# Kernel tuning notes

Measured on AMD Instinct MI355X. Metric: run time of the kernel, lower is better.

## Reference

```python
import jax, jax.numpy as jnp
import numpy as np

B, D_IN, D_H, N = 16, 32, 64, 4000
ORDER = 2
C_CAT = D_IN + D_H            # 96 channels into each gate conv
C_EFF = (ORDER + 1) * C_CAT   # 288 after order-K diffusion concat


def setup_inputs() -> dict:
    key = jax.random.key(0)
    ks = jax.random.split(key, 9)
    x = jax.random.normal(ks[0], (B, D_IN, N), dtype=jnp.float32)
    h = jax.random.normal(ks[1], (B, D_H, N), dtype=jnp.float32)
    # uniform adjacency, roughly row-normalized to keep diffusion stable
    adj = jax.random.uniform(ks[2], (N, N), dtype=jnp.float32) / N
    scale = 0.05
    Wf = jax.random.normal(ks[3], (D_H, C_EFF), dtype=jnp.float32) * scale
    Wu = jax.random.normal(ks[4], (D_H, C_EFF), dtype=jnp.float32) * scale
    Wc = jax.random.normal(ks[5], (D_H, C_EFF), dtype=jnp.float32) * scale
    bf = jax.random.normal(ks[6], (D_H,), dtype=jnp.float32) * scale
    bu = jax.random.normal(ks[7], (D_H,), dtype=jnp.float32) * scale
    bc = jax.random.normal(ks[8], (D_H,), dtype=jnp.float32) * scale
    return {"x": x, "h": h, "adj": adj, "Wf": Wf, "bf": bf,
            "Wu": Wu, "bu": bu, "Wc": Wc, "bc": bc}


def _spatial_conv(z, adj, W, b):
    # z: [b, c, n]; order-2 diffusion: concat [z, A z, A^2 z] then 1x1 conv
    z1 = jnp.einsum('mn,bcn->bcm', adj, z)
    z2 = jnp.einsum('mn,bcn->bcm', adj, z1)
    feats = jnp.concatenate([z, z1, z2], axis=1)           # [b, 3c, n]
    return jnp.einsum('oc,bcn->bon', W, feats) + b[None, :, None]


def reference(x, h, adj, Wf, bf, Wu, bu, Wc, bc):
    x_gates = jnp.concatenate([x, h], axis=1)              # [b, d_in+d_h, n]
    r = jax.nn.sigmoid(_spatial_conv(x_gates, adj, Wf, bf))
    u = jax.nn.sigmoid(_spatial_conv(x_gates, adj, Wu, bu))
    x_c = jnp.concatenate([x, r * h], axis=1)
    c = jnp.tanh(_spatial_conv(x_c, adj, Wc, bc))
    return u * h + (1.0 - u) * c
```

## Files before the change

kernel.cpp:

```cpp
#include <hip/hip_runtime.h>
#include <cstdint>


#define NREAL 4000
#define NPAD  4096

typedef unsigned short u16;
typedef __attribute__((ext_vector_type(8))) short short8;
typedef __attribute__((ext_vector_type(4))) float f32x4;
typedef __attribute__((ext_vector_type(4))) unsigned short u16x4;

__device__ __forceinline__ u16 f2bf(float f) {
  unsigned u = __builtin_bit_cast(unsigned, f);
  return (u16)((u + 0x7FFFu + ((u >> 16) & 1u)) >> 16);
}
__device__ __forceinline__ float bf2f(u16 b) {
  unsigned u = ((unsigned)b) << 16;
  return __builtin_bit_cast(float, u);
}

__global__ __launch_bounds__(256) void k_pack_adj(const float* __restrict__ adj,
                                                  u16* __restrict__ out) {
  const int idx = blockIdx.x * 256 + threadIdx.x;
  const int m = idx >> 10;
  const int n0 = (idx & 1023) << 2;
  u16x4 o;
  if (m < NREAL && n0 < NREAL) {
    const float4 v = *reinterpret_cast<const float4*>(&adj[(long)m * NREAL + n0]);
    o.x = f2bf(v.x); o.y = f2bf(v.y); o.z = f2bf(v.z); o.w = f2bf(v.w);
  } else {
    o.x = 0; o.y = 0; o.z = 0; o.w = 0;
  }
  *reinterpret_cast<u16x4*>(&out[(long)m * NPAD + n0]) = o;
}

__global__ __launch_bounds__(256) void k_pack_zg(const float* __restrict__ x,
                                                 const float* __restrict__ h,
                                                 u16* __restrict__ zg) {
  const int idx = blockIdx.x * 256 + threadIdx.x;
  const int row = idx >> 10;
  const int n0 = (idx & 1023) << 2;
  const int b = row / 96, c = row % 96;
  const float* src = (c < 32) ? &x[((long)b * 32 + c) * NREAL]
                              : &h[((long)b * 64 + (c - 32)) * NREAL];
  u16x4 o;
  if (n0 < NREAL) {
    const float4 v = *reinterpret_cast<const float4*>(&src[n0]);
    o.x = f2bf(v.x); o.y = f2bf(v.y); o.z = f2bf(v.z); o.w = f2bf(v.w);
  } else {
    o.x = 0; o.y = 0; o.z = 0; o.w = 0;
  }
  *reinterpret_cast<u16x4*>(&zg[(long)row * NPAD + n0]) = o;
}

__global__ __launch_bounds__(256) void k_pack_w(const float* __restrict__ Wf,
                                                const float* __restrict__ Wu,
                                                const float* __restrict__ Wc,
                                                float* __restrict__ Wgt,
                                                float* __restrict__ Wct) {
  const int idx = blockIdx.x * 256 + threadIdx.x;
  if (idx < 288 * 128) {
    const int c = idx >> 7, o = idx & 127;
    Wgt[idx] = (o < 64) ? Wf[o * 288 + c] : Wu[(o - 64) * 288 + c];
  }
  if (idx < 288 * 64) {
    const int c = idx >> 6, o = idx & 63;
    Wct[idx] = Wc[o * 288 + c];
  }
}

template<bool F32OUT>
__global__ __launch_bounds__(512, 2) void k_gemm256(const u16* __restrict__ A,
                                                    const u16* __restrict__ B,
                                                    void* __restrict__ Cout,
                                                    int ktPerChunk, long chunkElems) {
  __shared__ __align__(16) u16 As[2][256 * 64];
  __shared__ __align__(16) u16 Bs[2][256 * 64];
  const int tid = threadIdx.x;
  const int lane = tid & 63;
  const int wv = tid >> 6;
  const int wm = wv >> 2;
  const int wn = wv & 3;
  const int bm = blockIdx.y, bn = blockIdx.x;

  const int srow = tid >> 3;
  const int jlog = (tid & 7) ^ (srow & 7);
  const long kt0ofs = (long)blockIdx.z * ktPerChunk * 64;
  const u16* aS = A + (long)(bm * 256 + srow) * NPAD + kt0ofs + jlog * 8;
  const u16* bS = B + (long)(bn * 256 + srow) * NPAD + kt0ofs + jlog * 8;
  const int ldst = tid * 8;

  const int fr = lane & 15;
  const int ksub2 = ((lane >> 4) << 3) << 1;

  f32x4 acc[8][4] = {};

#define STAGE(buf, kk)                                                           \
  {                                                                              \
    const long ko = (long)(kk) * 64;                                             \
    _Pragma("unroll")                                                            \
    for (int i = 0; i < 4; ++i)                                                  \
      __builtin_amdgcn_global_load_lds(                                          \
          (const __attribute__((address_space(1))) void*)(aS + (long)i * 64 * NPAD + ko), \
          (__attribute__((address_space(3))) void*)(&As[buf][i * 4096 + ldst]), 16, 0, 0); \
    _Pragma("unroll")                                                            \
    for (int i = 0; i < 4; ++i)                                                  \
      __builtin_amdgcn_global_load_lds(                                          \
          (const __attribute__((address_space(1))) void*)(bS + (long)i * 64 * NPAD + ko), \
          (__attribute__((address_space(3))) void*)(&Bs[buf][i * 4096 + ldst]), 16, 0, 0); \
  }

  STAGE(0, 0)
  int cur = 0;
  for (int kk = 0; kk < ktPerChunk; ++kk) {
    if (kk + 1 < ktPerChunk) {
      STAGE(cur ^ 1, kk + 1)
      asm volatile("s_waitcnt vmcnt(8)\ns_barrier" ::: "memory");
    } else {
      asm volatile("s_waitcnt vmcnt(0)\ns_barrier" ::: "memory");
    }
    const char* Ab = (const char*)&As[cur][0];
    const char* Bb = (const char*)&Bs[cur][0];
#pragma unroll
    for (int ks = 0; ks < 2; ++ks) {
      const int k2 = (ks << 6) + ksub2;
      short8 av[8], bv[4];
#pragma unroll
      for (int mi = 0; mi < 8; ++mi) {
        const int row = (wm << 7) + (mi << 4) + fr;
        av[mi] = *(const short8*)(Ab + row * 128 + (k2 ^ ((row & 7) << 4)));
      }
#pragma unroll
      for (int ni = 0; ni < 4; ++ni) {
        const int row = (wn << 6) + (ni << 4) + fr;
        bv[ni] = *(const short8*)(Bb + row * 128 + (k2 ^ ((row & 7) << 4)));
      }
      __builtin_amdgcn_s_setprio(1);
#pragma unroll
      for (int mi = 0; mi < 8; ++mi)
#pragma unroll
        for (int ni = 0; ni < 4; ++ni)
          acc[mi][ni] = __builtin_amdgcn_mfma_f32_16x16x32_bf16(av[mi], bv[ni],
                                                                acc[mi][ni], 0, 0, 0);
      __builtin_amdgcn_s_setprio(0);
    }
    asm volatile("s_barrier" ::: "memory");
    cur ^= 1;
  }
#undef STAGE

  const int rb = bm * 256 + (wm << 7) + ((lane >> 4) << 2);
  const int cb = bn * 256 + (wn << 6) + fr;
  if (F32OUT) {
    float* C = (float*)Cout + (long)blockIdx.z * chunkElems;
#pragma unroll
    for (int mi = 0; mi < 8; ++mi)
#pragma unroll
      for (int ni = 0; ni < 4; ++ni)
#pragma unroll
        for (int q = 0; q < 4; ++q)
          C[(long)(rb + (mi << 4) + q) * NPAD + cb + (ni << 4)] = acc[mi][ni][q];
  } else {
    u16* C = (u16*)Cout;
#pragma unroll
    for (int mi = 0; mi < 8; ++mi)
#pragma unroll
      for (int ni = 0; ni < 4; ++ni)
#pragma unroll
        for (int q = 0; q < 4; ++q)
          C[(long)(rb + (mi << 4) + q) * NPAD + cb + (ni << 4)] = f2bf(acc[mi][ni][q]);
  }
}

template<int NC>
__global__ __launch_bounds__(256) void k_combine(const float* __restrict__ P,
                                                 long chunkElems,
                                                 u16* __restrict__ out) {
  const long i4 = ((long)blockIdx.x * 256 + threadIdx.x) * 4;
  f32x4 s = *reinterpret_cast<const f32x4*>(&P[i4]);
#pragma unroll
  for (int c = 1; c < NC; ++c) {
    const f32x4 v = *reinterpret_cast<const f32x4*>(&P[(long)c * chunkElems + i4]);
    s.x += v.x; s.y += v.y; s.z += v.z; s.w += v.w;
  }
  u16x4 o;
  o.x = f2bf(s.x); o.y = f2bf(s.y); o.z = f2bf(s.z); o.w = f2bf(s.w);
  *reinterpret_cast<u16x4*>(&out[i4]) = o;
}

__global__ __launch_bounds__(512) void k_gates(
    const float* __restrict__ x, const float* __restrict__ h,
    const float* __restrict__ Wgt,
    const float* __restrict__ bfv, const float* __restrict__ buv,
    const u16* __restrict__ Z1, const u16* __restrict__ Z2,
    u16* __restrict__ rh_bf, float* __restrict__ rh_f, float* __restrict__ u_f) {
  const int lane = threadIdx.x & 63;
  const int wq = __builtin_amdgcn_readfirstlane(threadIdx.x >> 6);
  const int b = blockIdx.y;
  const int n0 = blockIdx.x * 128 + (lane << 1);
  if (n0 >= NREAL) return;
  const int ob = wq << 4;
  const float* xb = x + (long)b * 32 * NREAL + n0;
  const float* hb = h + (long)b * 64 * NREAL + n0;
  const u16* z1b = Z1 + (long)b * 96 * NPAD + n0;
  const u16* z2b = Z2 + (long)b * 96 * NPAD + n0;

  float a0[16] = {}, a1[16] = {};
#pragma unroll 4
  for (int c = 0; c < 32; ++c) {
    const float2 f = *reinterpret_cast<const float2*>(&xb[(long)c * NREAL]);
#pragma unroll
    for (int oi = 0; oi < 16; ++oi) {
      const float w = Wgt[c * 128 + ob + oi];
      a0[oi] = fmaf(w, f.x, a0[oi]); a1[oi] = fmaf(w, f.y, a1[oi]);
    }
  }
#pragma unroll 4
  for (int c = 0; c < 64; ++c) {
    const float2 f = *reinterpret_cast<const float2*>(&hb[(long)c * NREAL]);
#pragma unroll
    for (int oi = 0; oi < 16; ++oi) {
      const float w = Wgt[(32 + c) * 128 + ob + oi];
      a0[oi] = fmaf(w, f.x, a0[oi]); a1[oi] = fmaf(w, f.y, a1[oi]);
    }
  }
#pragma unroll 4
  for (int c = 0; c < 96; ++c) {
    const unsigned pv = *reinterpret_cast<const unsigned*>(&z1b[(long)c * NPAD]);
    const float f0 = bf2f((u16)(pv & 0xffff)), f1 = bf2f((u16)(pv >> 16));
#pragma unroll
    for (int oi = 0; oi < 16; ++oi) {
      const float w = Wgt[(96 + c) * 128 + ob + oi];
      a0[oi] = fmaf(w, f0, a0[oi]); a1[oi] = fmaf(w, f1, a1[oi]);
    }
  }
#pragma unroll 4
  for (int c = 0; c < 96; ++c) {
    const unsigned pv = *reinterpret_cast<const unsigned*>(&z2b[(long)c * NPAD]);
    const float f0 = bf2f((u16)(pv & 0xffff)), f1 = bf2f((u16)(pv >> 16));
#pragma unroll
    for (int oi = 0; oi < 16; ++oi) {
      const float w = Wgt[(192 + c) * 128 + ob + oi];
      a0[oi] = fmaf(w, f0, a0[oi]); a1[oi] = fmaf(w, f1, a1[oi]);
    }
  }

  if (wq < 4) {
#pragma unroll
    for (int oi = 0; oi < 16; ++oi) {
      const int og = ob + oi;
      const float bb = bfv[og];
      const float r0 = 1.f / (1.f + __expf(-(a0[oi] + bb)));
      const float r1 = 1.f / (1.f + __expf(-(a1[oi] + bb)));
      const float2 hv = *reinterpret_cast<const float2*>(&hb[(long)og * NREAL]);
      const float rh0 = r0 * hv.x, rh1 = r1 * hv.y;
      if (rh_f)
        *reinterpret_cast<float2*>(&rh_f[((long)b * 64 + og) * NREAL + n0]) =
            make_float2(rh0, rh1);
      const unsigned pk = (unsigned)f2bf(rh0) | ((unsigned)f2bf(rh1) << 16);
      *reinterpret_cast<unsigned*>(&rh_bf[((long)b * 64 + og) * NPAD + n0]) = pk;
    }
  } else {
#pragma unroll
    for (int oi = 0; oi < 16; ++oi) {
      const int og = (ob - 64) + oi;
      const float bb = buv[og];
      const float u0 = 1.f / (1.f + __expf(-(a0[oi] + bb)));
      const float u1 = 1.f / (1.f + __expf(-(a1[oi] + bb)));
      *reinterpret_cast<float2*>(&u_f[((long)b * 64 + og) * NREAL + n0]) =
          make_float2(u0, u1);
    }
  }
}

template<bool RHF32>
__global__ __launch_bounds__(512) void k_cand(
    const float* __restrict__ x, const float* __restrict__ h,
    const float* __restrict__ Wct, const float* __restrict__ bcv,
    const u16* __restrict__ Z1, const u16* __restrict__ Z2,
    const u16* __restrict__ Rhb, const u16* __restrict__ Rh1,
    const u16* __restrict__ Rh2,
    const float* __restrict__ rh_f, const float* __restrict__ u_f,
    float* __restrict__ out) {
  const int lane = threadIdx.x & 63;
  const int wq = __builtin_amdgcn_readfirstlane(threadIdx.x >> 6);
  const int ob = (wq & 3) << 4;
  const int n = blockIdx.x * 128 + ((wq >> 2) << 6) + lane;
  const int b = blockIdx.y;
  if (n >= NREAL) return;
  const float* xb = x + (long)b * 32 * NREAL + n;
  const float* hb = h + (long)b * 64 * NREAL + n;
  const u16* z1b = Z1 + (long)b * 96 * NPAD + n;
  const u16* z2b = Z2 + (long)b * 96 * NPAD + n;
  const u16* r1b = Rh1 + (long)b * 64 * NPAD + n;
  const u16* r2b = Rh2 + (long)b * 64 * NPAD + n;
  const float* rfb = rh_f + (long)b * 64 * NREAL + n;
  const u16* rbb = Rhb + (long)b * 64 * NPAD + n;

  float acc[16] = {};
#pragma unroll 4
  for (int c = 0; c < 32; ++c) {
    const float f = xb[(long)c * NREAL];
#pragma unroll
    for (int oi = 0; oi < 16; ++oi)
      acc[oi] = fmaf(Wct[c * 64 + ob + oi], f, acc[oi]);
  }
#pragma unroll 4
  for (int c = 0; c < 64; ++c) {
    const float f = RHF32 ? rfb[(long)c * NREAL] : bf2f(rbb[(long)c * NPAD]);
#pragma unroll
    for (int oi = 0; oi < 16; ++oi)
      acc[oi] = fmaf(Wct[(32 + c) * 64 + ob + oi], f, acc[oi]);
  }
#pragma unroll 4
  for (int c = 0; c < 32; ++c) {
    const float f = bf2f(z1b[(long)c * NPAD]);
#pragma unroll
    for (int oi = 0; oi < 16; ++oi)
      acc[oi] = fmaf(Wct[(96 + c) * 64 + ob + oi], f, acc[oi]);
  }
#pragma unroll 4
  for (int c = 0; c < 64; ++c) {
    const float f = bf2f(r1b[(long)c * NPAD]);
#pragma unroll
    for (int oi = 0; oi < 16; ++oi)
      acc[oi] = fmaf(Wct[(128 + c) * 64 + ob + oi], f, acc[oi]);
  }
#pragma unroll 4
  for (int c = 0; c < 32; ++c) {
    const float f = bf2f(z2b[(long)c * NPAD]);
#pragma unroll
    for (int oi = 0; oi < 16; ++oi)
      acc[oi] = fmaf(Wct[(192 + c) * 64 + ob + oi], f, acc[oi]);
  }
#pragma unroll 4
  for (int c = 0; c < 64; ++c) {
    const float f = bf2f(r2b[(long)c * NPAD]);
#pragma unroll
    for (int oi = 0; oi < 16; ++oi)
      acc[oi] = fmaf(Wct[(224 + c) * 64 + ob + oi], f, acc[oi]);
  }

#pragma unroll
  for (int oi = 0; oi < 16; ++oi) {
    const int og = ob + oi;
    float v = acc[oi] + bcv[og];
    v = fminf(fmaxf(v, -15.f), 15.f);
    const float e2 = __expf(2.f * v);
    const float cv = (e2 - 1.f) / (e2 + 1.f);
    const float u = u_f[((long)b * 64 + og) * NREAL + n];
    out[((long)b * 64 + og) * NREAL + n] = u * hb[(long)og * NREAL] + (1.f - u) * cv;
  }
}

extern "C" void kernel_launch(void* const* d_in, const int* in_sizes, int n_in,
                              void* d_out, int out_size, void* d_ws, size_t ws_size,
                              hipStream_t stream) {
  const float* x   = (const float*)d_in[0];
  const float* h   = (const float*)d_in[1];
  const float* adj = (const float*)d_in[2];
  const float* Wf  = (const float*)d_in[3];
  const float* bf_ = (const float*)d_in[4];
  const float* Wu  = (const float*)d_in[5];
  const float* bu_ = (const float*)d_in[6];
  const float* Wc  = (const float*)d_in[7];
  const float* bc_ = (const float*)d_in[8];
  float* out = (float*)d_out;

  char* p = (char*)d_ws;
  auto alloc = [&](size_t bytes) { char* r = p; p += bytes; return r; };
  u16* adjb = (u16*)alloc((size_t)NPAD * NPAD * 2);
  u16* Zg   = (u16*)alloc((size_t)1536 * NPAD * 2);
  u16* Rhb  = Zg;
  u16* Z1   = (u16*)alloc((size_t)1536 * NPAD * 2);
  u16* Z2   = (u16*)alloc((size_t)1536 * NPAD * 2);
  u16* Rh1  = (u16*)alloc((size_t)1024 * NPAD * 2);
  u16* Rh2  = (u16*)alloc((size_t)1024 * NPAD * 2);
  float* uf = (float*)alloc((size_t)16 * 64 * NREAL * 4);
  float* Wgt = (float*)alloc(288 * 128 * 4);
  float* Wct = (float*)alloc(288 * 64 * 4);
  const size_t RHFB = (size_t)16 * 64 * NREAL * 4;
  size_t used = (size_t)(p - (char*)d_ws);
  float* rhf = nullptr;
  if (ws_size >= used + RHFB) rhf = (float*)alloc(RHFB);
  used = (size_t)(p - (char*)d_ws);

  const size_t PZ2 = (size_t)2 * 1536 * NPAD * 4;
  const size_t PR4 = (size_t)4 * 1024 * NPAD * 4;
  int sZ = 1, sR = 1;
  float* P = nullptr;
  if (ws_size >= used + PR4)      { P = (float*)alloc(PR4); sZ = 2; sR = 4; }
  else if (ws_size >= used + PZ2) { P = (float*)alloc(PZ2); sZ = 2; sR = 2; }

  auto gemm = [&](const u16* Ax, const u16* Bx, u16* Cb, int M, int sk) {
    const long ce = (long)M * NPAD;
    const int mt = M / 256;
    const int kpc = 64 / sk;
    if (sk == 4) {
      k_gemm256<true><<<dim3(16, mt, 4), 512, 0, stream>>>(Ax, Bx, P, kpc, ce);
      k_combine<4><<<dim3(M * 4), 256, 0, stream>>>(P, ce, Cb);
    } else if (sk == 2) {
      k_gemm256<true><<<dim3(16, mt, 2), 512, 0, stream>>>(Ax, Bx, P, kpc, ce);
      k_combine<2><<<dim3(M * 4), 256, 0, stream>>>(P, ce, Cb);
    } else {
      k_gemm256<false><<<dim3(16, mt, 1), 512, 0, stream>>>(Ax, Bx, Cb, 64, ce);
    }
  };

  k_pack_adj<<<dim3(NPAD * (NPAD / 4) / 256), 256, 0, stream>>>(adj, adjb);
  k_pack_zg <<<dim3(1536 * (NPAD / 4) / 256), 256, 0, stream>>>(x, h, Zg);
  k_pack_w  <<<dim3(144), 256, 0, stream>>>(Wf, Wu, Wc, Wgt, Wct);
  gemm(Zg, adjb, Z1, 1536, sZ);
  gemm(Z1, adjb, Z2, 1536, sZ);
  k_gates<<<dim3(32, 16), 512, 0, stream>>>(x, h, Wgt, bf_, bu_, Z1, Z2,
                                            Rhb, rhf, uf);
  gemm(Rhb, adjb, Rh1, 1024, sR);
  gemm(Rh1, adjb, Rh2, 1024, sR);
  if (rhf)
    k_cand<true><<<dim3(32, 16), 512, 0, stream>>>(x, h, Wct, bc_, Z1, Z2, Rhb,
                                                   Rh1, Rh2, rhf, uf, out);
  else
    k_cand<false><<<dim3(32, 16), 512, 0, stream>>>(x, h, Wct, bc_, Z1, Z2, Rhb,
                                                    Rh1, Rh2, rhf, uf, out);
}
```

Before: 495.1 us.

## Interleave next-tile global->LDS loads with MFMA phases in GEMM mainloop

```diff
diff --git a/kernel.cpp b/kernel.cpp
--- a/kernel.cpp
+++ b/kernel.cpp
@@ -69,6 +69,11 @@
   }
 }
 
+#define GLDS(dst, src)                                                         \
+  __builtin_amdgcn_global_load_lds(                                            \
+      (const __attribute__((address_space(1))) void*)(src),                    \
+      (__attribute__((address_space(3))) void*)(dst), 16, 0, 0)
+
 template<bool F32OUT>
 __global__ __launch_bounds__(512, 2) void k_gemm256(const u16* __restrict__ A,
                                                     const u16* __restrict__ B,
@@ -81,76 +86,98 @@
   const int wv = tid >> 6;
   const int wm = wv >> 2;
   const int wn = wv & 3;
-  const int bm = blockIdx.y, bn = blockIdx.x;
 
   const int srow = tid >> 3;
   const int jlog = (tid & 7) ^ (srow & 7);
-  const long kt0ofs = (long)blockIdx.z * ktPerChunk * 64;
-  const u16* aS = A + (long)(bm * 256 + srow) * NPAD + kt0ofs + jlog * 8;
-  const u16* bS = B + (long)(bn * 256 + srow) * NPAD + kt0ofs + jlog * 8;
+  const long kt0 = (long)blockIdx.z * ktPerChunk * 64;
+  const u16* aB = A + (long)(blockIdx.y * 256 + srow) * NPAD + kt0 + jlog * 8;
+  const u16* bB = B + (long)(blockIdx.x * 256 + srow) * NPAD + kt0 + jlog * 8;
   const int ldst = tid * 8;
 
   const int fr = lane & 15;
-  const int ksub2 = ((lane >> 4) << 3) << 1;
+  const int swz = (fr & 7) << 4;
+  const int kb0 = (((lane >> 4) << 4)) ^ swz;
+  const int kb1 = (64 + ((lane >> 4) << 4)) ^ swz;
 
   f32x4 acc[8][4] = {};
-
-#define STAGE(buf, kk)                                                           \
-  {                                                                              \
-    const long ko = (long)(kk) * 64;                                             \
-    _Pragma("unroll")                                                            \
-    for (int i = 0; i < 4; ++i)                                                  \
-      __builtin_amdgcn_global_load_lds(                                          \
-          (const __attribute__((address_space(1))) void*)(aS + (long)i * 64 * NPAD + ko), \
-          (__attribute__((address_space(3))) void*)(&As[buf][i * 4096 + ldst]), 16, 0, 0); \
-    _Pragma("unroll")                                                            \
-    for (int i = 0; i < 4; ++i)                                                  \
-      __builtin_amdgcn_global_load_lds(                                          \
-          (const __attribute__((address_space(1))) void*)(bS + (long)i * 64 * NPAD + ko), \
-          (__attribute__((address_space(3))) void*)(&Bs[buf][i * 4096 + ldst]), 16, 0, 0); \
-  }
-
-  STAGE(0, 0)
-  int cur = 0;
-  for (int kk = 0; kk < ktPerChunk; ++kk) {
-    if (kk + 1 < ktPerChunk) {
-      STAGE(cur ^ 1, kk + 1)
-      asm volatile("s_waitcnt vmcnt(8)\ns_barrier" ::: "memory");
-    } else {
-      asm volatile("s_waitcnt vmcnt(0)\ns_barrier" ::: "memory");
-    }
-    const char* Ab = (const char*)&As[cur][0];
-    const char* Bb = (const char*)&Bs[cur][0];
-#pragma unroll
-    for (int ks = 0; ks < 2; ++ks) {
-      const int k2 = (ks << 6) + ksub2;
-      short8 av[8], bv[4];
-#pragma unroll
-      for (int mi = 0; mi < 8; ++mi) {
-        const int row = (wm << 7) + (mi << 4) + fr;
-        av[mi] = *(const short8*)(Ab + row * 128 + (k2 ^ ((row & 7) << 4)));
+  const int T = ktPerChunk;
+
+  GLDS(&Bs[0][0 + ldst],     bB);
+  GLDS(&Bs[0][4096 + ldst],  bB + 64L * NPAD);
+  GLDS(&Bs[0][8192 + ldst],  bB + 128L * NPAD);
+  GLDS(&Bs[0][12288 + ldst], bB + 192L * NPAD);
+  GLDS(&As[0][0 + ldst],     aB);
+  GLDS(&As[0][8192 + ldst],  aB + 128L * NPAD);
+  GLDS(&As[0][4096 + ldst],  aB + 64L * NPAD);
+  GLDS(&As[0][12288 + ldst], aB + 192L * NPAD);
+  asm volatile("s_waitcnt vmcnt(0)" ::: "memory");
+  __builtin_amdgcn_s_barrier();
+  __builtin_amdgcn_sched_barrier(0);
+
+  for (int t = 0; t < T; ++t) {
+    const int bsel = t & 1;
+    const char* Ab = (const char*)&As[bsel][0];
+    const char* Bb = (const char*)&Bs[bsel][0];
+    u16* An = &As[bsel ^ 1][0];
+    u16* Bn = &Bs[bsel ^ 1][0];
+    const bool more = (t + 1 < T);
+    const long ko = (long)(t + 1) * 64;
+    short8 bv[4][2];
+#pragma unroll
+    for (int p = 0; p < 4; ++p) {
+      if (more) {
+        if (p == 0) { GLDS(Bn + ldst, bB + ko);
+                      GLDS(Bn + 4096 + ldst, bB + 64L * NPAD + ko); }
+        if (p == 1) { GLDS(Bn + 8192 + ldst, bB + 128L * NPAD + ko);
+                      GLDS(Bn + 12288 + ldst, bB + 192L * NPAD + ko); }
+        if (p == 2) { GLDS(An + ldst, aB + ko);
+                      GLDS(An + 8192 + ldst, aB + 128L * NPAD + ko); }
+        if (p == 3) { GLDS(An + 4096 + ldst, aB + 64L * NPAD + ko);
+                      GLDS(An + 12288 + ldst, aB + 192L * NPAD + ko); }
       }
-#pragma unroll
-      for (int ni = 0; ni < 4; ++ni) {
-        const int row = (wn << 6) + (ni << 4) + fr;
-        bv[ni] = *(const short8*)(Bb + row * 128 + (k2 ^ ((row & 7) << 4)));
+      asm volatile("" ::: "memory");
+      if (p == 0) {
+#pragma unroll
+        for (int ni = 0; ni < 4; ++ni) {
+          const int brow = (wn << 6) + (ni << 4) + fr;
+          bv[ni][0] = *(const short8*)(Bb + brow * 128 + kb0);
+          bv[ni][1] = *(const short8*)(Bb + brow * 128 + kb1);
+        }
+      }
+      short8 av[2][2];
+#pragma unroll
+      for (int q = 0; q < 2; ++q) {
+        const int arow = (wm << 7) + ((2 * p + q) << 4) + fr;
+        av[q][0] = *(const short8*)(Ab + arow * 128 + kb0);
+        av[q][1] = *(const short8*)(Ab + arow * 128 + kb1);
       }
       __builtin_amdgcn_s_setprio(1);
 #pragma unroll
-      for (int mi = 0; mi < 8; ++mi)
-#pragma unroll
-        for (int ni = 0; ni < 4; ++ni)
-          acc[mi][ni] = __builtin_amdgcn_mfma_f32_16x16x32_bf16(av[mi], bv[ni],
-                                                                acc[mi][ni], 0, 0, 0);
+      for (int q = 0; q < 2; ++q)
+#pragma unroll
+        for (int ni = 0; ni < 4; ++ni) {
+          acc[2 * p + q][ni] = __builtin_amdgcn_mfma_f32_16x16x32_bf16(
+              av[q][0], bv[ni][0], acc[2 * p + q][ni], 0, 0, 0);
+          acc[2 * p + q][ni] = __builtin_amdgcn_mfma_f32_16x16x32_bf16(
+              av[q][1], bv[ni][1], acc[2 * p + q][ni], 0, 0, 0);
+        }
       __builtin_amdgcn_s_setprio(0);
-    }
-    asm volatile("s_barrier" ::: "memory");
-    cur ^= 1;
-  }
-#undef STAGE
-
-  const int rb = bm * 256 + (wm << 7) + ((lane >> 4) << 2);
-  const int cb = bn * 256 + (wn << 6) + fr;
+      if (p == 1) {
+        if (more) asm volatile("s_waitcnt vmcnt(4)" ::: "memory");
+        else      asm volatile("s_waitcnt vmcnt(0)" ::: "memory");
+        __builtin_amdgcn_s_barrier();
+        __builtin_amdgcn_sched_barrier(0);
+      }
+      if (p == 3 && more) {
+        asm volatile("s_waitcnt vmcnt(2)" ::: "memory");
+        __builtin_amdgcn_s_barrier();
+        __builtin_amdgcn_sched_barrier(0);
+      }
+    }
+  }
+
+  const int rb = blockIdx.y * 256 + (wm << 7) + ((lane >> 4) << 2);
+  const int cb = blockIdx.x * 256 + (wn << 6) + fr;
   if (F32OUT) {
     float* C = (float*)Cout + (long)blockIdx.z * chunkElems;
 #pragma unroll
```

Measured after the change: 544.6 us. 10.0% more time.
